# Kernel optimization log

Hardware: AMD Instinct MI355X
Metric: run time of the kernel (lower is better)

The kernel has to match this reference:

```python
import jax, jax.numpy as jnp
import numpy as np

N_E = 1024
E_DIM = 256
BETA = 0.25


def setup_inputs() -> dict:
    key = jax.random.key(0)
    k1, k2 = jax.random.split(key)
    z = jax.random.normal(k1, (16, E_DIM, 64, 64), dtype=jnp.float32)
    # nn.Embedding weight initialized uniform(-1/n_e, 1/n_e)
    codebook = jax.random.uniform(k2, (N_E, E_DIM), dtype=jnp.float32,
                                  minval=-1.0 / N_E, maxval=1.0 / N_E)
    return {"z": z, "codebook": codebook}


def reference(z, codebook):
    B, C, H, W = z.shape
    zp = jnp.transpose(z, (0, 2, 3, 1))              # [B,H,W,C]
    zf = zp.reshape(-1, C)                           # [N, e_dim]
    d = (jnp.sum(zf * zf, axis=1, keepdims=True)
         + jnp.sum(codebook * codebook, axis=1)
         - 2.0 * zf @ codebook.T)                    # [N, n_e]
    idx = jnp.argmin(d, axis=1)                      # [N]
    # one-hot @ codebook == direct gather
    z_q = codebook[idx].reshape(zp.shape)            # [B,H,W,C]

    e_latent_loss = jnp.mean((jax.lax.stop_gradient(z_q) - zp) ** 2)
    q_latent_loss = jnp.mean((z_q - jax.lax.stop_gradient(zp)) ** 2)
    codebook_loss = q_latent_loss + BETA * e_latent_loss

    # straight-through estimator
    z_q_st = zp + jax.lax.stop_gradient(z_q - zp)
    out = jnp.transpose(z_q_st, (0, 3, 1, 2))        # [B,C,H,W]
    indices = idx.reshape(B, 1, H, W)
    return out, codebook_loss, indices
```

## Files before the change

### kernel.cpp

```cpp
#include <hip/hip_runtime.h>

#define NB 16
#define NC 256
#define NH 64
#define NW 64
#define NK 1024
#define HW (NH * NW)
#define NPOS (NB * HW)
#define NOUT (NB * NC * HW)
#define NSLOT 256

__device__ __forceinline__ float sq_rn(float x) { return __fmul_rn(x, x); }

__device__ __forceinline__ float pairwise_sumsq_256(const float* __restrict__ a,
                                                    int stride) {
    float s_half[2];
#pragma unroll
    for (int h = 0; h < 2; ++h) {
        const float* base = a + (size_t)(h * 128) * stride;
        float r[8];
#pragma unroll
        for (int j = 0; j < 8; ++j) r[j] = sq_rn(base[(size_t)j * stride]);
        for (int i = 8; i < 128; i += 8) {
#pragma unroll
            for (int j = 0; j < 8; ++j)
                r[j] = __fadd_rn(r[j], sq_rn(base[(size_t)(i + j) * stride]));
        }
        s_half[h] = __fadd_rn(
            __fadd_rn(__fadd_rn(r[0], r[1]), __fadd_rn(r[2], r[3])),
            __fadd_rn(__fadd_rn(r[4], r[5]), __fadd_rn(r[6], r[7])));
    }
    return __fadd_rn(s_half[0], s_half[1]);
}

__global__ __launch_bounds__(256) void cnorm_kernel(const float* __restrict__ cb,
                                                    float* __restrict__ cnorm) {
    int k = blockIdx.x * 256 + threadIdx.x;
    if (k < NK) {
        cnorm[k] = pairwise_sumsq_256(cb + (size_t)k * NC, 1);
    }
}

__global__ __launch_bounds__(256) void transpose_cb_kernel(const float* __restrict__ cb,
                                                           float* __restrict__ cbT) {
    const int k = blockIdx.x;
    const int d = threadIdx.x;
    cbT[(size_t)d * NK + k] = cb[(size_t)k * NC + d];
}

__global__ __launch_bounds__(512, 2) void argmin_kernel(const float* __restrict__ z,
                                                        const float* __restrict__ cbT,
                                                        const float* __restrict__ cnorm,
                                                        int* __restrict__ idx_ws,
                                                        float* __restrict__ idx_out) {
    __shared__ float z_lds[256][64];
    __shared__ float znorm_s[64];
    __shared__ float red_v[8][64];
    __shared__ int   red_i[8][64];

    const int blk = blockIdx.x;
    const int b = blk >> 6;
    const int hw0 = (blk & 63) * 64;
    const int t = threadIdx.x;
    const int lane = t & 63;
    const int wave = t >> 6;
    const int pg = lane & 7;
    const int cg = lane >> 3;

    const float* zg = z + (size_t)b * (NC * HW) + hw0;

#pragma unroll
    for (int i = 0; i < 8; ++i) {
        const int flat4 = i * 2048 + t * 4;
        const int d = flat4 >> 6;
        const int p = flat4 & 63;
        const float4 v = *(const float4*)(zg + (size_t)d * HW + p);
        *(float4*)&z_lds[d][p] = v;
    }
    if (wave == 0) znorm_s[lane] = pairwise_sumsq_256(zg + lane, HW);
    __syncthreads();

    float best[8];
    int bid[8];
#pragma unroll
    for (int i = 0; i < 8; ++i) { best[i] = 3.4e38f; bid[i] = 0; }

#pragma unroll 1
    for (int pass = 0; pass < 2; ++pass) {
        float acc[8][8];
#pragma unroll
        for (int i = 0; i < 8; ++i)
#pragma unroll
            for (int j = 0; j < 8; ++j) acc[i][j] = 0.f;

        const int k0 = wave * 128 + pass * 64 + cg * 8;
        const float* cp = cbT + k0;

#pragma unroll 1
        for (int it = 0; it < 64; ++it) {
            const int ds = it * 4;
            float4 cbuf[8];
#pragma unroll
            for (int q = 0; q < 8; ++q)
                cbuf[q] = *(const float4*)(cp + (size_t)(ds + (q >> 1)) * NK
                                              + (q & 1) * 4);
#pragma unroll
            for (int dl = 0; dl < 4; ++dl) {
                const int d = ds + dl;
                const float4 za = *(const float4*)&z_lds[d][pg * 8];
                const float4 zb = *(const float4*)&z_lds[d][pg * 8 + 4];
                const float zf[8] = {za.x, za.y, za.z, za.w,
                                     zb.x, zb.y, zb.z, zb.w};
                const float4 ca = cbuf[dl * 2];
                const float4 cc = cbuf[dl * 2 + 1];
                const float cf[8] = {ca.x, ca.y, ca.z, ca.w,
                                     cc.x, cc.y, cc.z, cc.w};
#pragma unroll
                for (int i = 0; i < 8; ++i)
#pragma unroll
                    for (int j = 0; j < 8; ++j)
                        acc[i][j] = __fmaf_rn(zf[i], cf[j], acc[i][j]);
            }
        }

        const float4 cn0 = *(const float4*)(cnorm + k0);
        const float4 cn1 = *(const float4*)(cnorm + k0 + 4);
        const float cnf[8] = {cn0.x, cn0.y, cn0.z, cn0.w,
                              cn1.x, cn1.y, cn1.z, cn1.w};
        float znl[8];
#pragma unroll
        for (int i = 0; i < 8; ++i) znl[i] = znorm_s[pg * 8 + i];
#pragma unroll
        for (int j = 0; j < 8; ++j) {
            const int k = k0 + j;
#pragma unroll
            for (int i = 0; i < 8; ++i) {
                const float sc = __fsub_rn(__fadd_rn(znl[i], cnf[j]),
                                           __fmul_rn(2.0f, acc[i][j]));
                if (sc < best[i]) { best[i] = sc; bid[i] = k; }
            }
        }
    }

#pragma unroll
    for (int off = 32; off >= 8; off >>= 1) {
#pragma unroll
        for (int i = 0; i < 8; ++i) {
            const float v = __shfl_down(best[i], off, 64);
            const int d2 = __shfl_down(bid[i], off, 64);
            if (v < best[i] || (v == best[i] && d2 < bid[i])) {
                best[i] = v;
                bid[i] = d2;
            }
        }
    }
    if (cg == 0) {
#pragma unroll
        for (int i = 0; i < 8; ++i) {
            red_v[wave][pg * 8 + i] = best[i];
            red_i[wave][pg * 8 + i] = bid[i];
        }
    }
    __syncthreads();

    if (t < 64) {
        float bv = red_v[0][t];
        int bi = red_i[0][t];
#pragma unroll
        for (int w = 1; w < 8; ++w) {
            const float v = red_v[w][t];
            const int i2 = red_i[w][t];
            if (v < bv || (v == bv && i2 < bi)) { bv = v; bi = i2; }
        }
        const int g = b * HW + hw0 + t;
        idx_ws[g] = bi;
        idx_out[g] = (float)bi;
    }
}

__global__ __launch_bounds__(256) void gather_loss_kernel(const float* __restrict__ z,
                                                          const float* __restrict__ cb,
                                                          const int* __restrict__ idx_ws,
                                                          float* __restrict__ out,
                                                          double* __restrict__ loss_acc) {
    const unsigned g = blockIdx.x * 256u + threadIdx.x;
    const unsigned e = g * 4u;
    const unsigned w = e & 63u;
    const unsigned h = (e >> 6) & 63u;
    const unsigned c = (e >> 12) & 255u;
    const unsigned b = e >> 20;

    const unsigned p = b * HW + h * NW + w;

    const int4 iv = *(const int4*)(idx_ws + p);
    const float4 z4 = *(const float4*)(z + e);

    float4 o;
    o.x = cb[(size_t)iv.x * NC + c];
    o.y = cb[(size_t)iv.y * NC + c];
    o.z = cb[(size_t)iv.z * NC + c];
    o.w = cb[(size_t)iv.w * NC + c];

    *(float4*)(out + e) = o;

    const float d0 = o.x - z4.x;
    const float d1 = o.y - z4.y;
    const float d2 = o.z - z4.z;
    const float d3 = o.w - z4.w;
    float part = d0 * d0 + d1 * d1 + d2 * d2 + d3 * d3;

#pragma unroll
    for (int off = 32; off > 0; off >>= 1) part += __shfl_down(part, off, 64);

    __shared__ float wsum[4];
    const int lane = threadIdx.x & 63;
    const int wave = threadIdx.x >> 6;
    if (lane == 0) wsum[wave] = part;
    __syncthreads();
    if (threadIdx.x == 0) {
        float s = wsum[0] + wsum[1] + wsum[2] + wsum[3];
        atomicAdd(loss_acc + (blockIdx.x & (NSLOT - 1)), (double)s);
    }
}

__global__ void finalize_kernel(const double* __restrict__ loss_acc,
                                float* __restrict__ out_loss) {
    if (threadIdx.x == 0) {
        double s = 0.0;
        for (int i = 0; i < NSLOT; ++i) s += loss_acc[i];
        *out_loss = (float)(1.25 * s / (double)NOUT);
    }
}

extern "C" void kernel_launch(void* const* d_in, const int* in_sizes, int n_in,
                              void* d_out, int out_size, void* d_ws, size_t ws_size,
                              hipStream_t stream) {
    const float* z = (const float*)d_in[0];
    const float* cb = (const float*)d_in[1];

    float* out = (float*)d_out;
    float* loss_out = out + NOUT;
    float* idx_out = out + NOUT + 1;

    double* loss_acc = (double*)d_ws;
    float* cnorm = (float*)((char*)d_ws + 2048);
    int* idx_ws = (int*)((char*)d_ws + 2048 + 4096);
    float* cbT = (float*)((char*)d_ws + 2048 + 4096 + NPOS * 4);

    hipMemsetAsync(d_ws, 0, 2048, stream);
    cnorm_kernel<<<(NK + 255) / 256, 256, 0, stream>>>(cb, cnorm);
    transpose_cb_kernel<<<NK, 256, 0, stream>>>(cb, cbT);
    argmin_kernel<<<NPOS / 64, 512, 0, stream>>>(z, cbT, cnorm, idx_ws, idx_out);
    gather_loss_kernel<<<NOUT / 1024, 256, 0, stream>>>(z, cb, idx_ws, out, loss_acc);
    finalize_kernel<<<1, 64, 0, stream>>>(loss_acc, loss_out);
}
```

Before: 621.9 us.

## Fuse gather and loss into argmin kernel, repack codebook as d4-interleaved layout

```diff
diff --git a/kernel.cpp b/kernel.cpp
--- a/kernel.cpp
+++ b/kernel.cpp
@@ -41,18 +41,20 @@
     }
 }
 
-__global__ __launch_bounds__(256) void transpose_cb_kernel(const float* __restrict__ cb,
-                                                           float* __restrict__ cbT) {
+__global__ __launch_bounds__(256) void pack_cb_kernel(const float* __restrict__ cb,
+                                                      float* __restrict__ cbT2) {
     const int k = blockIdx.x;
     const int d = threadIdx.x;
-    cbT[(size_t)d * NK + k] = cb[(size_t)k * NC + d];
+    cbT2[(size_t)((d >> 2) * NK + k) * 4 + (d & 3)] = cb[(size_t)k * NC + d];
 }
 
 __global__ __launch_bounds__(512, 2) void argmin_kernel(const float* __restrict__ z,
-                                                        const float* __restrict__ cbT,
+                                                        const float* __restrict__ cb,
+                                                        const float* __restrict__ cbT2,
                                                         const float* __restrict__ cnorm,
-                                                        int* __restrict__ idx_ws,
-                                                        float* __restrict__ idx_out) {
+                                                        float* __restrict__ out,
+                                                        float* __restrict__ idx_out,
+                                                        double* __restrict__ loss_acc) {
     __shared__ float z_lds[256][64];
     __shared__ float znorm_s[64];
     __shared__ float red_v[8][64];
@@ -94,32 +96,28 @@
             for (int j = 0; j < 8; ++j) acc[i][j] = 0.f;
 
         const int k0 = wave * 128 + pass * 64 + cg * 8;
-        const float* cp = cbT + k0;
+        const float* cp2 = cbT2 + (size_t)k0 * 4;
 
 #pragma unroll 1
         for (int it = 0; it < 64; ++it) {
-            const int ds = it * 4;
             float4 cbuf[8];
 #pragma unroll
             for (int q = 0; q < 8; ++q)
-                cbuf[q] = *(const float4*)(cp + (size_t)(ds + (q >> 1)) * NK
-                                              + (q & 1) * 4);
+                cbuf[q] = *(const float4*)(cp2 + (size_t)it * 4096 + q * 4);
 #pragma unroll
             for (int dl = 0; dl < 4; ++dl) {
-                const int d = ds + dl;
+                const int d = it * 4 + dl;
                 const float4 za = *(const float4*)&z_lds[d][pg * 8];
                 const float4 zb = *(const float4*)&z_lds[d][pg * 8 + 4];
                 const float zf[8] = {za.x, za.y, za.z, za.w,
                                      zb.x, zb.y, zb.z, zb.w};
-                const float4 ca = cbuf[dl * 2];
-                const float4 cc = cbuf[dl * 2 + 1];
-                const float cf[8] = {ca.x, ca.y, ca.z, ca.w,
-                                     cc.x, cc.y, cc.z, cc.w};
 #pragma unroll
                 for (int i = 0; i < 8; ++i)
 #pragma unroll
                     for (int j = 0; j < 8; ++j)
-                        acc[i][j] = __fmaf_rn(zf[i], cf[j], acc[i][j]);
+                        acc[i][j] = __fmaf_rn(zf[i],
+                                              ((const float*)&cbuf[j])[dl],
+                                              acc[i][j]);
             }
         }
 
@@ -172,54 +170,44 @@
             const int i2 = red_i[w][t];
             if (v < bv || (v == bv && i2 < bi)) { bv = v; bi = i2; }
         }
-        const int g = b * HW + hw0 + t;
-        idx_ws[g] = bi;
-        idx_out[g] = (float)bi;
-    }
-}
-
-__global__ __launch_bounds__(256) void gather_loss_kernel(const float* __restrict__ z,
-                                                          const float* __restrict__ cb,
-                                                          const int* __restrict__ idx_ws,
-                                                          float* __restrict__ out,
-                                                          double* __restrict__ loss_acc) {
-    const unsigned g = blockIdx.x * 256u + threadIdx.x;
-    const unsigned e = g * 4u;
-    const unsigned w = e & 63u;
-    const unsigned h = (e >> 6) & 63u;
-    const unsigned c = (e >> 12) & 255u;
-    const unsigned b = e >> 20;
-
-    const unsigned p = b * HW + h * NW + w;
-
-    const int4 iv = *(const int4*)(idx_ws + p);
-    const float4 z4 = *(const float4*)(z + e);
-
-    float4 o;
-    o.x = cb[(size_t)iv.x * NC + c];
-    o.y = cb[(size_t)iv.y * NC + c];
-    o.z = cb[(size_t)iv.z * NC + c];
-    o.w = cb[(size_t)iv.w * NC + c];
-
-    *(float4*)(out + e) = o;
-
-    const float d0 = o.x - z4.x;
-    const float d1 = o.y - z4.y;
-    const float d2 = o.z - z4.z;
-    const float d3 = o.w - z4.w;
-    float part = d0 * d0 + d1 * d1 + d2 * d2 + d3 * d3;
-
-#pragma unroll
-    for (int off = 32; off > 0; off >>= 1) part += __shfl_down(part, off, 64);
-
-    __shared__ float wsum[4];
-    const int lane = threadIdx.x & 63;
-    const int wave = threadIdx.x >> 6;
-    if (lane == 0) wsum[wave] = part;
-    __syncthreads();
-    if (threadIdx.x == 0) {
-        float s = wsum[0] + wsum[1] + wsum[2] + wsum[3];
-        atomicAdd(loss_acc + (blockIdx.x & (NSLOT - 1)), (double)s);
+        idx_out[b * HW + hw0 + t] = (float)bi;
+        red_i[0][t] = bi;
+    }
+    __syncthreads();
+
+    float* outg = out + (size_t)b * (NC * HW) + hw0;
+    float lsum = 0.f;
+#pragma unroll 1
+    for (int r = 0; r < 8; ++r) {
+        const int id = r * 512 + t;
+        const int c = id >> 4;
+        const int p4 = (id & 15) * 4;
+        const int i0 = red_i[0][p4];
+        const int i1 = red_i[0][p4 + 1];
+        const int i2 = red_i[0][p4 + 2];
+        const int i3 = red_i[0][p4 + 3];
+        float4 o;
+        o.x = cb[(size_t)i0 * NC + c];
+        o.y = cb[(size_t)i1 * NC + c];
+        o.z = cb[(size_t)i2 * NC + c];
+        o.w = cb[(size_t)i3 * NC + c];
+        *(float4*)(outg + (size_t)c * HW + p4) = o;
+        const float4 zv = *(const float4*)&z_lds[c][p4];
+        const float d0 = o.x - zv.x;
+        const float d1 = o.y - zv.y;
+        const float d2 = o.z - zv.z;
+        const float d3 = o.w - zv.w;
+        lsum += d0 * d0 + d1 * d1 + d2 * d2 + d3 * d3;
+    }
+#pragma unroll
+    for (int off = 32; off > 0; off >>= 1) lsum += __shfl_down(lsum, off, 64);
+    if (lane == 0) red_v[wave][0] = lsum;
+    __syncthreads();
+    if (t == 0) {
+        float s = 0.f;
+#pragma unroll
+        for (int w = 0; w < 8; ++w) s += red_v[w][0];
+        atomicAdd(loss_acc + (blk & (NSLOT - 1)), (double)s);
     }
 }
 
@@ -244,13 +232,12 @@
 
     double* loss_acc = (double*)d_ws;
     float* cnorm = (float*)((char*)d_ws + 2048);
-    int* idx_ws = (int*)((char*)d_ws + 2048 + 4096);
-    float* cbT = (float*)((char*)d_ws + 2048 + 4096 + NPOS * 4);
+    float* cbT2 = (float*)((char*)d_ws + 2048 + 4096);
 
     hipMemsetAsync(d_ws, 0, 2048, stream);
     cnorm_kernel<<<(NK + 255) / 256, 256, 0, stream>>>(cb, cnorm);
-    transpose_cb_kernel<<<NK, 256, 0, stream>>>(cb, cbT);
-    argmin_kernel<<<NPOS / 64, 512, 0, stream>>>(z, cbT, cnorm, idx_ws, idx_out);
-    gather_loss_kernel<<<NOUT / 1024, 256, 0, stream>>>(z, cb, idx_ws, out, loss_acc);
+    pack_cb_kernel<<<NK, 256, 0, stream>>>(cb, cbT2);
+    argmin_kernel<<<NPOS / 64, 512, 0, stream>>>(z, cb, cbT2, cnorm,
+                                                 out, idx_out, loss_acc);
     finalize_kernel<<<1, 64, 0, stream>>>(loss_acc, loss_out);
 }
```

New measurement: 580.3 us. 1.07x faster.
